# Optimization experiments

Measured on AMD Instinct MI355X. Metric: run time of the kernel, lower is better.

Reference implementation:

```python
import jax, jax.numpy as jnp
import numpy as np

B, S, F = 128, 1024, 512
H = 32          # LSTM hidden size
G = 4 * H       # i, f, g, o gates


def setup_inputs() -> dict:
    key = jax.random.key(0)
    ks = jax.random.split(key, 12)
    sc = lambda fan_in: 1.0 / np.sqrt(fan_in)
    return {
        "x":  jax.random.normal(ks[0], (B, S, F), dtype=jnp.float32),
        "W1": jax.random.normal(ks[1], (F, 32), dtype=jnp.float32) * sc(F),
        "b1": jnp.zeros((32,), jnp.float32),
        "W2": jax.random.normal(ks[2], (32, 64), dtype=jnp.float32) * sc(32),
        "b2": jnp.zeros((64,), jnp.float32),
        "Wx": jax.random.normal(ks[3], (64, G), dtype=jnp.float32) * sc(64),
        "Wh": jax.random.normal(ks[4], (H, G), dtype=jnp.float32) * sc(H),
        "bl": jnp.zeros((G,), jnp.float32),
        "W3": jax.random.normal(ks[5], (H, 64), dtype=jnp.float32) * sc(H),
        "b3": jnp.zeros((64,), jnp.float32),
        "W4": jax.random.normal(ks[6], (64, 512), dtype=jnp.float32) * sc(64),
        "b4": jnp.zeros((512,), jnp.float32),
    }


def _lstm_scan(xg, Wh):
    # xg: [B, S, 4H] precomputed input-side gate pre-activations (incl. bias)
    def step(carry, xt):
        c, h = carry
        g = xt + h @ Wh                      # [B, 4H]
        i, f, gg, o = jnp.split(g, 4, axis=-1)
        i, f, o = jax.nn.sigmoid(i), jax.nn.sigmoid(f), jax.nn.sigmoid(o)
        c = f * c + i * jnp.tanh(gg)
        h = o * jnp.tanh(c)
        return (c, h), h

    c0 = jnp.zeros((xg.shape[0], H), xg.dtype)
    h0 = jnp.zeros((xg.shape[0], H), xg.dtype)
    _, hs = jax.lax.scan(step, (c0, h0), jnp.swapaxes(xg, 0, 1))  # hs: [S, B, H]
    return jnp.swapaxes(hs, 0, 1)            # [B, S, H]


def reference(x, W1, b1, W2, b2, Wx, Wh, bl, W3, b3, W4, b4):
    h = jnp.tanh(x @ W1 + b1)                # [B, S, 32]
    h = jnp.tanh(h @ W2 + b2)                # [B, S, 64]
    xg = h @ Wx + bl                          # [B, S, 4H] input-side gates
    hs = _lstm_scan(xg, Wh)                   # [B, S, H]
    h = jnp.tanh(hs @ W3 + b3)                # [B, S, 64]
    return h @ W4 + b4                        # [B, S, 512]
```

## Files before the change

kernel.cpp:

```cpp
#include <hip/hip_runtime.h>
#include <hip/hip_bf16.h>


typedef __attribute__((ext_vector_type(8))) __bf16 bf16x8;
typedef __attribute__((ext_vector_type(4))) __bf16 bf16x4;
typedef __attribute__((ext_vector_type(4))) float floatx4;

__global__ __launch_bounds__(256) void k_mlp_xg(
    const float* __restrict__ x,  const float* __restrict__ W1, const float* __restrict__ b1,
    const float* __restrict__ W2, const float* __restrict__ b2,
    const float* __restrict__ Wx, const float* __restrict__ bl,
    float* __restrict__ xg)
{
    __shared__ __align__(16) char smem[51712];
    __bf16* w1T = (__bf16*)smem;
    __bf16* w2T = (__bf16*)smem;
    __bf16* wxT = (__bf16*)(smem + 5120);
    __bf16* xsh = (__bf16*)(smem + 33280);
    __bf16* xsl = (__bf16*)(smem + 42496);
    __bf16* h1s = (__bf16*)(smem + 33280);
    __bf16* h2s = (__bf16*)(smem + 38400);

    const int tid  = threadIdx.x;
    const int lane = tid & 63, w = tid >> 6;
    const int quad = lane >> 4, col = lane & 15;
    const int row0 = blockIdx.x * 64;
    const int m     = w * 16 + col;
    const int rbase = w * 16 + quad * 4;
    const floatx4 fzero = {0.f, 0.f, 0.f, 0.f};

    for (int i = tid; i < 512 * 32; i += 256) {
        int k = i >> 5, n = i & 31;
        w1T[n * 520 + k] = (__bf16)W1[i];
    }
    auto stage_x = [&](int kc) {
        for (int i4 = tid; i4 < 1024; i4 += 256) {
            int f = i4 << 2; int r = f >> 6, cc = f & 63;
            float4 v = *(const float4*)(x + (size_t)(row0 + r) * 512 + kc * 64 + cc);
            __bf16 h0 = (__bf16)v.x, h1 = (__bf16)v.y, h2 = (__bf16)v.z, h3 = (__bf16)v.w;
            bf16x4 hi = {h0, h1, h2, h3};
            bf16x4 lo = {(__bf16)(v.x - (float)h0), (__bf16)(v.y - (float)h1),
                         (__bf16)(v.z - (float)h2), (__bf16)(v.w - (float)h3)};
            *(bf16x4*)(xsh + r * 72 + cc) = hi;
            *(bf16x4*)(xsl + r * 72 + cc) = lo;
        }
    };
    stage_x(0);
    __syncthreads();

    floatx4 acc1[2] = {fzero, fzero};
    for (int kc = 0; kc < 8; ++kc) {
#pragma unroll
        for (int ks = 0; ks < 2; ++ks) {
            int ko = ks * 32 + quad * 8;
            bf16x8 ah = *(const bf16x8*)(xsh + m * 72 + ko);
            bf16x8 al = *(const bf16x8*)(xsl + m * 72 + ko);
            int kg = kc * 64 + ko;
#pragma unroll
            for (int nt = 0; nt < 2; ++nt) {
                bf16x8 bfr = *(const bf16x8*)(w1T + (nt * 16 + col) * 520 + kg);
                acc1[nt] = __builtin_amdgcn_mfma_f32_16x16x32_bf16(ah, bfr, acc1[nt], 0, 0, 0);
                acc1[nt] = __builtin_amdgcn_mfma_f32_16x16x32_bf16(al, bfr, acc1[nt], 0, 0, 0);
            }
        }
        if (kc < 7) { __syncthreads(); stage_x(kc + 1); __syncthreads(); }
    }
    __syncthreads();

#pragma unroll
    for (int nt = 0; nt < 2; ++nt) {
        float bb = b1[nt * 16 + col];
#pragma unroll
        for (int r = 0; r < 4; ++r)
            h1s[(rbase + r) * 40 + nt * 16 + col] = (__bf16)tanhf(acc1[nt][r] + bb);
    }
    for (int i = tid; i < 32 * 64; i += 256)  { int k = i >> 6, n = i & 63;  w2T[n * 40 + k] = (__bf16)W2[i]; }
    for (int i = tid; i < 64 * 128; i += 256) { int k = i >> 7, n = i & 127; wxT[n * 72 + k] = (__bf16)Wx[i]; }
    __syncthreads();

    bf16x8 a2 = *(const bf16x8*)(h1s + m * 40 + quad * 8);
    floatx4 acc2[4];
#pragma unroll
    for (int nt = 0; nt < 4; ++nt) {
        bf16x8 bfr = *(const bf16x8*)(w2T + (nt * 16 + col) * 40 + quad * 8);
        acc2[nt] = __builtin_amdgcn_mfma_f32_16x16x32_bf16(a2, bfr, fzero, 0, 0, 0);
    }
#pragma unroll
    for (int nt = 0; nt < 4; ++nt) {
        float bb = b2[nt * 16 + col];
#pragma unroll
        for (int r = 0; r < 4; ++r)
            h2s[(rbase + r) * 72 + nt * 16 + col] = (__bf16)tanhf(acc2[nt][r] + bb);
    }

    floatx4 acc3[8];
#pragma unroll
    for (int nt = 0; nt < 8; ++nt) acc3[nt] = fzero;
#pragma unroll
    for (int ks = 0; ks < 2; ++ks) {
        int ko = ks * 32 + quad * 8;
        bf16x8 a3 = *(const bf16x8*)(h2s + m * 72 + ko);
#pragma unroll
        for (int nt = 0; nt < 8; ++nt) {
            bf16x8 bfr = *(const bf16x8*)(wxT + (nt * 16 + col) * 72 + ko);
            acc3[nt] = __builtin_amdgcn_mfma_f32_16x16x32_bf16(a3, bfr, acc3[nt], 0, 0, 0);
        }
    }
#pragma unroll
    for (int nt = 0; nt < 8; ++nt) {
        float bb = bl[nt * 16 + col];
#pragma unroll
        for (int r = 0; r < 4; ++r)
            xg[(size_t)(row0 + rbase + r) * 128 + nt * 16 + col] = acc3[nt][r] + bb;
    }
}

#define RLANE(v, k) __uint_as_float(__builtin_amdgcn_readlane(__float_as_uint(v), (k)))

__global__ __launch_bounds__(64) void k_lstm(
    const float* __restrict__ xg, const float* __restrict__ Wh,
    float* __restrict__ hs)
{
    const int b = blockIdx.x;
    const int l = threadIdx.x;
    const float* xgb = xg + (size_t)b * 1024 * 128;
    float* hsb = hs + (size_t)b * 1024 * 32;

    float whA[32], whB[32];
#pragma unroll
    for (int k = 0; k < 32; ++k) {
        whA[k] = Wh[k * 128 + l];
        whB[k] = Wh[k * 128 + 64 + l];
    }
    const float sc1 = (l < 32) ? 2.0f : 1.0f;
    const float m1  = (l < 32) ? 2.0f : 1.0f;
    const float c1  = (l < 32) ? -1.0f : 0.0f;

    float c = 0.f, h = 0.f;

    float xr0[4], xr1[4];
#pragma unroll
    for (int p = 0; p < 4; ++p) {
        xr0[p] = xgb[p * 128 + l];
        xr1[p] = xgb[p * 128 + 64 + l];
    }

    for (int t = 0; t < 1024; t += 4) {
#pragma unroll
        for (int u = 0; u < 4; ++u) {
            const int tc = t + u;
            float x0 = xr0[u], x1 = xr1[u];
            {
                int tp = tc + 4; tp = (tp > 1023) ? 1023 : tp;
                xr0[u] = xgb[tp * 128 + l];
                xr1[u] = xgb[tp * 128 + 64 + l];
            }
            float p0a = x0, p0b = 0.f, p0c = 0.f, p0d = 0.f;
            float p1a = x1, p1b = 0.f, p1c = 0.f, p1d = 0.f;
#pragma unroll
            for (int k = 0; k < 32; k += 4) {
                float h0 = RLANE(h, k);
                float h1 = RLANE(h, k + 1);
                float h2 = RLANE(h, k + 2);
                float h3 = RLANE(h, k + 3);
                p0a += h0 * whA[k];     p1a += h0 * whB[k];
                p0b += h1 * whA[k + 1]; p1b += h1 * whB[k + 1];
                p0c += h2 * whA[k + 2]; p1c += h2 * whB[k + 2];
                p0d += h3 * whA[k + 3]; p1d += h3 * whB[k + 3];
            }
            float pre0 = (p0a + p0b) + (p0c + p0d);
            float pre1 = (p1a + p1b) + (p1c + p1d);
            float a0 = __builtin_amdgcn_rcpf(1.0f + __expf(-pre0));
            float s1 = __builtin_amdgcn_rcpf(1.0f + __expf(-sc1 * pre1));
            float a1 = __builtin_fmaf(s1, m1, c1);
            float f_ = __shfl(a0, l ^ 32);
            float o_ = __shfl(a1, l ^ 32);
            c = f_ * c + a0 * a1;
            float e = __expf(-2.0f * c);
            float th = (1.0f - e) * __builtin_amdgcn_rcpf(1.0f + e);
            h = o_ * th;
            if (l < 32) hsb[tc * 32 + l] = h;
        }
    }
}

__global__ __launch_bounds__(256) void k_tail(
    const float* __restrict__ hs, const float* __restrict__ W3, const float* __restrict__ b3,
    const float* __restrict__ W4, const float* __restrict__ b4,
    float* __restrict__ out)
{
    __shared__ __align__(16) char smem[37888];
    __bf16* hss = (__bf16*)smem;
    __bf16* w3T = (__bf16*)(smem + 5120);
    __bf16* h3s = (__bf16*)(smem + 10240);
    __bf16* w4T = (__bf16*)(smem + 19456);

    const int tid  = threadIdx.x;
    const int lane = tid & 63, w = tid >> 6;
    const int quad = lane >> 4, col = lane & 15;
    const int row0 = blockIdx.x * 64;
    const int m     = w * 16 + col;
    const int rbase = w * 16 + quad * 4;
    const floatx4 fzero = {0.f, 0.f, 0.f, 0.f};

    for (int i4 = tid; i4 < 512; i4 += 256) {
        int f = i4 << 2; int r = f >> 5, cc = f & 31;
        float4 v = *(const float4*)(hs + (size_t)(row0 + r) * 32 + cc);
        bf16x4 hv = {(__bf16)v.x, (__bf16)v.y, (__bf16)v.z, (__bf16)v.w};
        *(bf16x4*)(hss + r * 40 + cc) = hv;
    }
    for (int i = tid; i < 32 * 64; i += 256) { int k = i >> 6, n = i & 63; w3T[n * 40 + k] = (__bf16)W3[i]; }
    __syncthreads();

    bf16x8 a3 = *(const bf16x8*)(hss + m * 40 + quad * 8);
    floatx4 acc3[4];
#pragma unroll
    for (int nt = 0; nt < 4; ++nt) {
        bf16x8 bfr = *(const bf16x8*)(w3T + (nt * 16 + col) * 40 + quad * 8);
        acc3[nt] = __builtin_amdgcn_mfma_f32_16x16x32_bf16(a3, bfr, fzero, 0, 0, 0);
    }
#pragma unroll
    for (int nt = 0; nt < 4; ++nt) {
        float bb = b3[nt * 16 + col];
#pragma unroll
        for (int r = 0; r < 4; ++r)
            h3s[(rbase + r) * 72 + nt * 16 + col] = (__bf16)tanhf(acc3[nt][r] + bb);
    }

    for (int oc = 0; oc < 4; ++oc) {
        __syncthreads();
        for (int i4 = tid; i4 < 2048; i4 += 256) {
            int f = i4 << 2; int k = f >> 7, cc = f & 127;
            float4 v = *(const float4*)(W4 + (size_t)k * 512 + oc * 128 + cc);
            w4T[(cc + 0) * 72 + k] = (__bf16)v.x;
            w4T[(cc + 1) * 72 + k] = (__bf16)v.y;
            w4T[(cc + 2) * 72 + k] = (__bf16)v.z;
            w4T[(cc + 3) * 72 + k] = (__bf16)v.w;
        }
        __syncthreads();

        floatx4 acc4[8];
#pragma unroll
        for (int nt = 0; nt < 8; ++nt) acc4[nt] = fzero;
#pragma unroll
        for (int ks = 0; ks < 2; ++ks) {
            int ko = ks * 32 + quad * 8;
            bf16x8 a4 = *(const bf16x8*)(h3s + m * 72 + ko);
#pragma unroll
            for (int nt = 0; nt < 8; ++nt) {
                bf16x8 bfr = *(const bf16x8*)(w4T + (nt * 16 + col) * 72 + ko);
                acc4[nt] = __builtin_amdgcn_mfma_f32_16x16x32_bf16(a4, bfr, acc4[nt], 0, 0, 0);
            }
        }
#pragma unroll
        for (int nt = 0; nt < 8; ++nt) {
            float bb = b4[oc * 128 + nt * 16 + col];
#pragma unroll
            for (int r = 0; r < 4; ++r)
                out[(size_t)(row0 + rbase + r) * 512 + oc * 128 + nt * 16 + col] = acc4[nt][r] + bb;
        }
    }
}

extern "C" void kernel_launch(void* const* d_in, const int* in_sizes, int n_in,
                              void* d_out, int out_size, void* d_ws, size_t ws_size,
                              hipStream_t stream)
{
    (void)in_sizes; (void)n_in; (void)out_size;
    const float* x  = (const float*)d_in[0];
    const float* W1 = (const float*)d_in[1];
    const float* b1 = (const float*)d_in[2];
    const float* W2 = (const float*)d_in[3];
    const float* b2 = (const float*)d_in[4];
    const float* Wx = (const float*)d_in[5];
    const float* Wh = (const float*)d_in[6];
    const float* bl = (const float*)d_in[7];
    const float* W3 = (const float*)d_in[8];
    const float* b3 = (const float*)d_in[9];
    const float* W4 = (const float*)d_in[10];
    const float* b4 = (const float*)d_in[11];
    float* out = (float*)d_out;

    const size_t hsElems = (size_t)128 * 1024 * 32;
    const size_t xgElems = (size_t)128 * 1024 * 128;
    float* hs = (float*)d_ws;
    float* xg = (ws_size >= (hsElems + xgElems) * sizeof(float))
                    ? hs + hsElems
                    : out;

    k_mlp_xg<<<2048, 256, 0, stream>>>(x, W1, b1, W2, b2, Wx, bl, xg);
    k_lstm<<<128, 64, 0, stream>>>(xg, Wh, hs);
    k_tail<<<2048, 256, 0, stream>>>(hs, W3, b3, W4, b4, out);
}
```

Measured before the change: 885.9 us.

## Stage LSTM gate inputs through triple-buffered LDS and use packed float2 FMAs

The LSTM recurrence kernel now prefetches 32-timestep chunks of the precomputed input gates into a three-deep LDS ring using global_load_lds, with explicit vmcnt waits. Per-step operands are read from LDS rather than from per-step global loads. The aim is to take global memory latency off the serial recurrence's critical path. The Wh-times-h dot product is also rewritten with float2 vectors so the compiler can emit packed FMAs. The risks are vmcnt counting that also picks up the hs stores, which could be fragile or over-wait, and the added LDS read latency on each step.

```diff
diff --git a/kernel.cpp b/kernel.cpp
--- a/kernel.cpp
+++ b/kernel.cpp
@@ -5,6 +5,7 @@
 typedef __attribute__((ext_vector_type(8))) __bf16 bf16x8;
 typedef __attribute__((ext_vector_type(4))) __bf16 bf16x4;
 typedef __attribute__((ext_vector_type(4))) float floatx4;
+typedef __attribute__((ext_vector_type(2))) float floatx2;
 
 __global__ __launch_bounds__(256) void k_mlp_xg(
     const float* __restrict__ x,  const float* __restrict__ W1, const float* __restrict__ b1,
@@ -121,65 +122,91 @@
     const float* __restrict__ xg, const float* __restrict__ Wh,
     float* __restrict__ hs)
 {
+    __shared__ __align__(16) float xbuf[3][32 * 128];
+
     const int b = blockIdx.x;
     const int l = threadIdx.x;
     const float* xgb = xg + (size_t)b * 1024 * 128;
     float* hsb = hs + (size_t)b * 1024 * 32;
 
-    float whA[32], whB[32];
-#pragma unroll
-    for (int k = 0; k < 32; ++k) {
-        whA[k] = Wh[k * 128 + l];
-        whB[k] = Wh[k * 128 + 64 + l];
-    }
+    floatx2 wh[32];
+#pragma unroll
+    for (int k = 0; k < 32; ++k)
+        wh[k] = floatx2{Wh[k * 128 + l], Wh[k * 128 + 64 + l]};
+
     const float sc1 = (l < 32) ? 2.0f : 1.0f;
     const float m1  = (l < 32) ? 2.0f : 1.0f;
     const float c1  = (l < 32) ? -1.0f : 0.0f;
 
+    auto stage_chunk = [&](int cidx) {
+        const float* src = xgb + (size_t)cidx * 4096 + l * 4;
+        float* dst = &xbuf[cidx % 3][0];
+#pragma unroll
+        for (int i = 0; i < 16; ++i)
+            __builtin_amdgcn_global_load_lds(src + i * 256, dst + i * 256, 16, 0, 0);
+    };
+
+    stage_chunk(0); stage_chunk(1); stage_chunk(2);
+    asm volatile("s_waitcnt vmcnt(16)" ::: "memory");
+
     float c = 0.f, h = 0.f;
 
     float xr0[4], xr1[4];
 #pragma unroll
     for (int p = 0; p < 4; ++p) {
-        xr0[p] = xgb[p * 128 + l];
-        xr1[p] = xgb[p * 128 + 64 + l];
-    }
-
-    for (int t = 0; t < 1024; t += 4) {
-#pragma unroll
-        for (int u = 0; u < 4; ++u) {
-            const int tc = t + u;
-            float x0 = xr0[u], x1 = xr1[u];
-            {
-                int tp = tc + 4; tp = (tp > 1023) ? 1023 : tp;
-                xr0[u] = xgb[tp * 128 + l];
-                xr1[u] = xgb[tp * 128 + 64 + l];
+        xr0[p] = xbuf[0][p * 128 + l];
+        xr1[p] = xbuf[0][p * 128 + 64 + l];
+    }
+
+#pragma unroll 1
+    for (int ch = 0; ch < 32; ++ch) {
+        const float* bufc = xbuf[ch % 3];
+        const float* bufn = xbuf[(ch + 1) % 3];
+#pragma unroll 1
+        for (int s = 0; s < 32; s += 4) {
+#pragma unroll
+            for (int u = 0; u < 4; ++u) {
+                const int tc = ch * 32 + s + u;
+                float x0 = xr0[u], x1 = xr1[u];
+                {
+                    int rn = s + u + 4;
+                    const float* p = (rn < 32) ? (bufc + rn * 128) : (bufn + (rn - 32) * 128);
+                    xr0[u] = p[l];
+                    xr1[u] = p[64 + l];
+                }
+                floatx2 pa = {x0, x1};
+                floatx2 pb = {0.f, 0.f}, pc = {0.f, 0.f}, pd = {0.f, 0.f};
+#pragma unroll
+                for (int k = 0; k < 32; k += 4) {
+                    float h0 = RLANE(h, k);
+                    float h1 = RLANE(h, k + 1);
+                    float h2 = RLANE(h, k + 2);
+                    float h3 = RLANE(h, k + 3);
+                    pa += wh[k]     * h0;
+                    pb += wh[k + 1] * h1;
+                    pc += wh[k + 2] * h2;
+                    pd += wh[k + 3] * h3;
+                }
+                floatx2 pe = (pa + pb) + (pc + pd);
+                float pre0 = pe.x;
+                float pre1 = pe.y;
+                float a0 = __builtin_amdgcn_rcpf(1.0f + __expf(-pre0));
+                float s1 = __builtin_amdgcn_rcpf(1.0f + __expf(-sc1 * pre1));
+                float a1 = __builtin_fmaf(s1, m1, c1);
+                float f_ = __shfl(a0, l ^ 32);
+                float o_ = __shfl(a1, l ^ 32);
+                c = f_ * c + a0 * a1;
+                float e = __expf(-2.0f * c);
+                float th = (1.0f - e) * __builtin_amdgcn_rcpf(1.0f + e);
+                h = o_ * th;
+                if (l < 32) hsb[tc * 32 + l] = h;
             }
-            float p0a = x0, p0b = 0.f, p0c = 0.f, p0d = 0.f;
-            float p1a = x1, p1b = 0.f, p1c = 0.f, p1d = 0.f;
-#pragma unroll
-            for (int k = 0; k < 32; k += 4) {
-                float h0 = RLANE(h, k);
-                float h1 = RLANE(h, k + 1);
-                float h2 = RLANE(h, k + 2);
-                float h3 = RLANE(h, k + 3);
-                p0a += h0 * whA[k];     p1a += h0 * whB[k];
-                p0b += h1 * whA[k + 1]; p1b += h1 * whB[k + 1];
-                p0c += h2 * whA[k + 2]; p1c += h2 * whB[k + 2];
-                p0d += h3 * whA[k + 3]; p1d += h3 * whB[k + 3];
-            }
-            float pre0 = (p0a + p0b) + (p0c + p0d);
-            float pre1 = (p1a + p1b) + (p1c + p1d);
-            float a0 = __builtin_amdgcn_rcpf(1.0f + __expf(-pre0));
-            float s1 = __builtin_amdgcn_rcpf(1.0f + __expf(-sc1 * pre1));
-            float a1 = __builtin_fmaf(s1, m1, c1);
-            float f_ = __shfl(a0, l ^ 32);
-            float o_ = __shfl(a1, l ^ 32);
-            c = f_ * c + a0 * a1;
-            float e = __expf(-2.0f * c);
-            float th = (1.0f - e) * __builtin_amdgcn_rcpf(1.0f + e);
-            h = o_ * th;
-            if (l < 32) hsb[tc * 32 + l] = h;
+        }
+        if (ch + 3 < 32) {
+            stage_chunk(ch + 3);
+            asm volatile("s_waitcnt vmcnt(16)" ::: "memory");
+        } else {
+            asm volatile("s_waitcnt vmcnt(0)" ::: "memory");
         }
     }
 }
```

Result: faster. 830.9 us (-6.2%).
